# Kernel tuning notes

Hardware: AMD Instinct MI355X
Metric: run time of the kernel (lower is better)

Reference implementation:

```python
import jax, jax.numpy as jnp
import numpy as np

N = 100_000   # nodes
E = 1_600_000 # edges (avg degree 16)
D = 128       # dim == dim_out
NEG_SLOPE = 0.2  # PyG GATConv default


def setup_inputs() -> dict:
    key = jax.random.key(0)
    ks = jax.random.split(key, 11)
    s = 1.0 / np.sqrt(D)
    return {
        "x": jax.random.normal(ks[0], (N, D), jnp.float32),
        "edge_index": jax.random.randint(ks[1], (2, E), 0, N, jnp.int32),
        "W1": jax.random.normal(ks[2], (D, D), jnp.float32) * s,
        "a_src1": jax.random.normal(ks[3], (D,), jnp.float32) * s,
        "a_dst1": jax.random.normal(ks[4], (D,), jnp.float32) * s,
        "b1": jnp.zeros((D,), jnp.float32),
        "W2": jax.random.normal(ks[5], (D, D), jnp.float32) * s,
        "a_src2": jax.random.normal(ks[6], (D,), jnp.float32) * s,
        "a_dst2": jax.random.normal(ks[7], (D,), jnp.float32) * s,
        "b2": jnp.zeros((D,), jnp.float32),
    }


def gat_conv(x, W, a_src, a_dst, b, src, dst, n):
    # PyG GATConv, heads=1: message flows src (j) -> dst (i)
    h = x @ W                              # [n, d]
    al_src = h @ a_src                     # per-node src attention logit
    al_dst = h @ a_dst                     # per-node dst attention logit
    e = jax.nn.leaky_relu(al_src[src] + al_dst[dst], NEG_SLOPE)  # [E']
    # softmax over incoming edges of each destination node (segment softmax)
    m = jax.ops.segment_max(e, dst, num_segments=n)
    e = jnp.exp(e - m[dst])
    z = jax.ops.segment_sum(e, dst, num_segments=n)
    alpha = e / z[dst]                     # [E']
    out = jax.ops.segment_sum(h[src] * alpha[:, None], dst, num_segments=n)
    return out + b


def reference(x, edge_index, W1, a_src1, a_dst1, b1, W2, a_src2, a_dst2, b2):
    n = x.shape[0]
    loop = jnp.arange(n, dtype=edge_index.dtype)
    src = jnp.concatenate([edge_index[0], loop])  # add_self_loops=True
    dst = jnp.concatenate([edge_index[1], loop])
    h = gat_conv(x, W1, a_src1, a_dst1, b1, src, dst, n)
    # self_loops=True -> residual=False; dropout in eval mode = identity
    return gat_conv(h, W2, a_src2, a_dst2, b2, src, dst, n)
```

## Files before the change

### kernel.cpp

```cpp
#include <hip/hip_runtime.h>
#include <hip/hip_bf16.h>
#include <math.h>

#define D 128
#define LRELU_SLOPE 0.2f
#define BSH 9
#define BSZ 512
#define SC_CHUNK 16384

typedef __attribute__((ext_vector_type(8))) short bf16x8;
typedef __attribute__((ext_vector_type(4))) float f32x4;

__device__ __forceinline__ float lrelu(float x){ return x > 0.f ? x : LRELU_SLOPE * x; }

__device__ __forceinline__ unsigned short bf16_rn(float x){
  unsigned int u = __float_as_uint(x);
  return (unsigned short)((u + 0x7FFFu + ((u >> 16) & 1u)) >> 16);
}
__device__ __forceinline__ float bf16_lo_f(unsigned int u){ return __uint_as_float(u << 16); }
__device__ __forceinline__ float bf16_hi_f(unsigned int u){ return __uint_as_float(u & 0xFFFF0000u); }

__global__ __launch_bounds__(1024) void bucket_count_kernel(const int* __restrict__ dst, int E,
    int* __restrict__ bcnt, int nbuck){
  __shared__ int h[256];
  int t = threadIdx.x;
  if (t < 256) h[t] = 0;
  __syncthreads();
  for (int e = blockIdx.x*1024 + t; e < E; e += gridDim.x*1024)
    atomicAdd(&h[dst[e] >> BSH], 1);
  __syncthreads();
  if (t < nbuck && h[t]) atomicAdd(&bcnt[t], h[t]);
}

__global__ __launch_bounds__(256) void bucket_scan_kernel(const int* __restrict__ bcnt,
    int* __restrict__ bbase, int* __restrict__ bcur, int nbuck, int E){
  __shared__ int s[256];
  int t = threadIdx.x;
  int v = (t < nbuck) ? bcnt[t] : 0;
  s[t] = v;
  __syncthreads();
  #pragma unroll
  for (int d = 1; d < 256; d <<= 1){
    int add = (t >= d) ? s[t-d] : 0;
    __syncthreads();
    s[t] += add;
    __syncthreads();
  }
  if (t < nbuck){ int b = s[t] - v; bbase[t] = b; bcur[t] = b; }
  if (t == 0) bbase[nbuck] = E;
}

__global__ __launch_bounds__(1024) void bucket_scatter_kernel(const int* __restrict__ src,
    const int* __restrict__ dst, int E, int* __restrict__ bcur,
    unsigned int* __restrict__ ebuf, int nbuck){
  __shared__ int h[256];
  __shared__ int cb[256];
  int t = threadIdx.x;
  int base = blockIdx.x * SC_CHUNK;
  int end = base + SC_CHUNK; if (end > E) end = E;
  if (t < 256) h[t] = 0;
  __syncthreads();
  for (int e = base + t; e < end; e += 1024)
    atomicAdd(&h[dst[e] >> BSH], 1);
  __syncthreads();
  if (t < nbuck){
    cb[t] = h[t] ? atomicAdd(&bcur[t], h[t]) : 0;
    h[t] = 0;
  }
  __syncthreads();
  for (int e = base + t; e < end; e += 1024){
    int d = dst[e];
    int b = d >> BSH;
    int lpos = atomicAdd(&h[b], 1);
    ebuf[cb[b] + lpos] = ((unsigned int)src[e] << BSH) | (unsigned int)(d & (BSZ-1));
  }
}

__global__ __launch_bounds__(256) void bucket_csr_kernel(const unsigned int* __restrict__ ebuf,
    const int* __restrict__ bbase, int* __restrict__ row_ptr, int* __restrict__ col,
    int n, int nbuck){
  __shared__ int c[512];
  __shared__ int ps[256];
  int b = blockIdx.x;
  int t = threadIdx.x;
  int base = bbase[b], end = bbase[b+1];
  c[t] = 0; c[t+256] = 0;
  __syncthreads();
  for (int i = base + t; i < end; i += 256)
    atomicAdd(&c[ebuf[i] & (BSZ-1)], 1);
  __syncthreads();
  int a0 = c[2*t], a1 = c[2*t+1];
  int pair = a0 + a1;
  ps[t] = pair;
  __syncthreads();
  #pragma unroll
  for (int d = 1; d < 256; d <<= 1){
    int add = (t >= d) ? ps[t-d] : 0;
    __syncthreads();
    ps[t] += add;
    __syncthreads();
  }
  int excl = ps[t] - pair;
  __syncthreads();
  int lo = b << BSH;
  int g0 = lo + 2*t, g1 = g0 + 1;
  if (g0 < n) row_ptr[g0] = base + excl;
  if (g1 < n) row_ptr[g1] = base + excl + a0;
  c[2*t]   = excl;
  c[2*t+1] = excl + a0;
  __syncthreads();
  for (int i = base + t; i < end; i += 256){
    unsigned int p = ebuf[i];
    int dlo = p & (BSZ-1);
    int pos = base + atomicAdd(&c[dlo], 1);
    col[pos] = (int)(p >> BSH);
  }
  if (b == 0 && t == 0) row_ptr[n] = bbase[nbuck];
}

__global__ __launch_bounds__(256) void wsplit_kernel(const float* __restrict__ W,
    unsigned short* __restrict__ Whf, unsigned short* __restrict__ Wlf){
  int t = blockIdx.x*256 + threadIdx.x;
  int k  = t >> 7;
  int nn = t & 127;
  float w = W[t];
  unsigned short h = bf16_rn(w);
  float whf = __uint_as_float(((unsigned int)h) << 16);
  unsigned short l = bf16_rn(w - whf);
  int kc = k >> 5, l4 = (k >> 3) & 3, e = k & 7;
  int cf = nn >> 4, l15 = nn & 15;
  int idx = ((kc*8 + cf)*64 + l4*16 + l15)*8 + e;
  Whf[idx] = h; Wlf[idx] = l;
}

__global__ __launch_bounds__(64) void wa_kernel(const float* __restrict__ W,
    const float* __restrict__ a_src, const float* __restrict__ a_dst,
    float* __restrict__ wa_s, float* __restrict__ wa_d){
  int task = blockIdx.x;
  int row = task & 127;
  const float* a = (task >> 7) ? a_dst : a_src;
  int l = threadIdx.x;
  float2 v = ((const float2*)(W + row*D))[l];
  float p = v.x*a[2*l] + v.y*a[2*l+1];
  #pragma unroll
  for (int off = 32; off >= 1; off >>= 1) p += __shfl_xor(p, off);
  if (l == 0) ((task >> 7) ? wa_d : wa_s)[row] = p;
}

__global__ __launch_bounds__(256) void wafrag_kernel(const float* __restrict__ wa_s,
    const float* __restrict__ wa_d, unsigned short* __restrict__ Whfx,
    unsigned short* __restrict__ Wlfx){
  int t = threadIdx.x;
  int kc = t >> 6, lane = t & 63;
  int l15 = lane & 15, l4 = lane >> 4;
  unsigned short hh[8], ll[8];
  #pragma unroll
  for (int e = 0; e < 8; ++e){
    int k = (kc*4 + l4)*8 + e;
    float v = (l15 == 0) ? wa_s[k] : ((l15 == 1) ? wa_d[k] : 0.f);
    unsigned short h = bf16_rn(v);
    hh[e] = h;
    ll[e] = bf16_rn(v - __uint_as_float(((unsigned)h) << 16));
  }
  #pragma unroll
  for (int e = 0; e < 8; ++e){ Whfx[t*8 + e] = hh[e]; Wlfx[t*8 + e] = ll[e]; }
}

__global__ __launch_bounds__(256) void gemm_al_kernel(const float* __restrict__ X,
    const unsigned short* __restrict__ Whf, const unsigned short* __restrict__ Wlf,
    const unsigned short* __restrict__ Whfx, const unsigned short* __restrict__ Wlfx,
    unsigned short* __restrict__ Hb, float* __restrict__ ALs, float* __restrict__ ALd, int n)
{
  __shared__ unsigned short Xh[128*128];
  int tid  = threadIdx.x;
  int lane = tid & 63;
  int wave = tid >> 6;
  int row0 = blockIdx.x * 128;
  int c4   = tid & 31;

  #pragma unroll 4
  for (int it = 0; it < 16; ++it){
    int f  = it*256 + tid;
    int r  = f >> 5;
    float4 v = make_float4(0.f,0.f,0.f,0.f);
    int gr = row0 + r;
    if (gr < n) v = ((const float4*)(X + (size_t)gr*D))[c4];
    unsigned short h0 = bf16_rn(v.x);
    unsigned short h1 = bf16_rn(v.y);
    unsigned short h2 = bf16_rn(v.z);
    unsigned short h3 = bf16_rn(v.w);
    int g   = (c4 >> 1) ^ (r & 7);
    int idx = r*128 + (g << 3) + ((c4 & 1) << 2);
    *(uint2*)&Xh[idx] = make_uint2((unsigned)h0 | ((unsigned)h1<<16),
                                   (unsigned)h2 | ((unsigned)h3<<16));
  }
  __syncthreads();

  int l15 = lane & 15;
  int l4  = lane >> 4;

  f32x4 acc[2][8];
  f32x4 acc2[2];
  #pragma unroll
  for (int rf = 0; rf < 2; ++rf){
    #pragma unroll
    for (int cf = 0; cf < 8; ++cf)
      acc[rf][cf] = (f32x4){0.f, 0.f, 0.f, 0.f};
    acc2[rf] = (f32x4){0.f, 0.f, 0.f, 0.f};
  }

  #pragma unroll
  for (int kc = 0; kc < 4; ++kc){
    int g = kc*4 + l4;
    bf16x8 ah[2];
    #pragma unroll
    for (int rf = 0; rf < 2; ++rf){
      int r   = wave*32 + rf*16 + l15;
      int idx = r*128 + ((g ^ (r & 7)) << 3);
      ah[rf] = *(const bf16x8*)&Xh[idx];
    }
    #pragma unroll
    for (int cf = 0; cf < 8; ++cf){
      int foff = ((kc*8 + cf) << 9) + (lane << 3);
      bf16x8 bh = *(const bf16x8*)&Whf[foff];
      bf16x8 bl = *(const bf16x8*)&Wlf[foff];
      #pragma unroll
      for (int rf = 0; rf < 2; ++rf){
        acc[rf][cf] = __builtin_amdgcn_mfma_f32_16x16x32_bf16(ah[rf], bh, acc[rf][cf], 0, 0, 0);
        acc[rf][cf] = __builtin_amdgcn_mfma_f32_16x16x32_bf16(ah[rf], bl, acc[rf][cf], 0, 0, 0);
      }
    }
    {
      int foffx = ((kc << 6) + lane) << 3;
      bf16x8 bhx = *(const bf16x8*)&Whfx[foffx];
      bf16x8 blx = *(const bf16x8*)&Wlfx[foffx];
      #pragma unroll
      for (int rf = 0; rf < 2; ++rf){
        acc2[rf] = __builtin_amdgcn_mfma_f32_16x16x32_bf16(ah[rf], bhx, acc2[rf], 0, 0, 0);
        acc2[rf] = __builtin_amdgcn_mfma_f32_16x16x32_bf16(ah[rf], blx, acc2[rf], 0, 0, 0);
      }
    }
  }

  #pragma unroll
  for (int rf = 0; rf < 2; ++rf){
    #pragma unroll
    for (int reg = 0; reg < 4; ++reg){
      int gr = row0 + wave*32 + rf*16 + l4*4 + reg;
      if (gr < n){
        unsigned int p0 = (unsigned)bf16_rn(acc[rf][0][reg]) | ((unsigned)bf16_rn(acc[rf][1][reg]) << 16);
        unsigned int p1 = (unsigned)bf16_rn(acc[rf][2][reg]) | ((unsigned)bf16_rn(acc[rf][3][reg]) << 16);
        unsigned int p2 = (unsigned)bf16_rn(acc[rf][4][reg]) | ((unsigned)bf16_rn(acc[rf][5][reg]) << 16);
        unsigned int p3 = (unsigned)bf16_rn(acc[rf][6][reg]) | ((unsigned)bf16_rn(acc[rf][7][reg]) << 16);
        ((uint4*)(Hb + (size_t)gr*D))[l15] = make_uint4(p0, p1, p2, p3);
        if (l15 == 0)      ALs[gr] = acc2[rf][reg];
        else if (l15 == 1) ALd[gr] = acc2[rf][reg];
      }
    }
  }
}

__global__ __launch_bounds__(256) void agg_kernel(const unsigned short* __restrict__ Hb,
    const float* __restrict__ ALs, const float* __restrict__ ALd,
    const int* __restrict__ row_ptr, const int* __restrict__ col,
    const float* __restrict__ bias, float* __restrict__ out, int n)
{
  __shared__ uint2 pairs[256];
  int gtid = blockIdx.x*blockDim.x + threadIdx.x;
  int node = gtid >> 6;
  int lane = threadIdx.x & 63;
  int wbase = threadIdx.x & 192;
  if (node >= n) return;

  int beg = row_ptr[node], end = row_ptr[node+1];
  float ald = ALd[node];
  float e_self = lrelu(ALs[node] + ald);

  const unsigned int* H2 = (const unsigned int*)Hb;
  unsigned int us = H2[(unsigned)(node*64 + lane)];
  float2 acc; acc.x = bf16_lo_f(us); acc.y = bf16_hi_f(us);
  float m = e_self, z = 1.f;

  for (int c = beg; c < end; c += 64){
    int j = c + lane;
    bool valid = j < end;
    int s_l = valid ? col[j] : 0;
    float e_l = valid ? lrelu(ALs[s_l] + ald) : -1e30f;

    float mc = e_l;
    #pragma unroll
    for (int off = 32; off >= 1; off >>= 1) mc = fmaxf(mc, __shfl_xor(mc, off));
    if (mc > m){
      float sc = __expf(m - mc);
      z *= sc; acc.x *= sc; acc.y *= sc;
      m = mc;
    }
    float w_l = valid ? __expf(e_l - m) : 0.f;
    float zs = w_l;
    #pragma unroll
    for (int off = 32; off >= 1; off >>= 1) zs += __shfl_xor(zs, off);
    z += zs;

    pairs[threadIdx.x] = make_uint2((unsigned)s_l, __float_as_uint(w_l));

    int cnt = end - c; if (cnt > 64) cnt = 64;
    int q = 0;
    for (; q + 8 <= cnt; q += 8){
      uint2 pw[8]; unsigned int u[8];
      #pragma unroll
      for (int p = 0; p < 8; ++p) pw[p] = pairs[wbase + q + p];
      #pragma unroll
      for (int p = 0; p < 8; ++p) u[p] = H2[(unsigned)(pw[p].x*64u + lane)];
      #pragma unroll
      for (int p = 0; p < 8; ++p){
        float w = __uint_as_float(pw[p].y);
        acc.x += w*bf16_lo_f(u[p]);
        acc.y += w*bf16_hi_f(u[p]);
      }
    }
    for (; q < cnt; ++q){
      uint2 pw = pairs[wbase + q];
      unsigned int u = H2[(unsigned)(pw.x*64u + lane)];
      float w = __uint_as_float(pw.y);
      acc.x += w*bf16_lo_f(u); acc.y += w*bf16_hi_f(u);
    }
  }

  float zi = 1.f / z;
  acc.x *= zi; acc.y *= zi;

  int q0 = (lane >> 4) + ((lane & 7) << 3);
  int q1 = q0 + 4;
  int hsel = (lane >> 3) & 1;
  float x0 = __shfl(acc.x, q0), y0 = __shfl(acc.y, q0);
  float x1 = __shfl(acc.x, q1), y1 = __shfl(acc.y, q1);
  float v0 = hsel ? y0 : x0;
  float v1 = hsel ? y1 : x1;

  float2 b2 = ((const float2*)bias)[lane];
  ((float2*)out)[(size_t)node*64 + lane] = make_float2(v0 + b2.x, v1 + b2.y);
}

extern "C" void kernel_launch(void* const* d_in, const int* in_sizes, int n_in,
                              void* d_out, int out_size, void* d_ws, size_t ws_size,
                              hipStream_t stream)
{
  const float* x   = (const float*)d_in[0];
  const int*   ei  = (const int*)  d_in[1];
  const float* W1  = (const float*)d_in[2];
  const float* as1 = (const float*)d_in[3];
  const float* ad1 = (const float*)d_in[4];
  const float* b1  = (const float*)d_in[5];
  const float* W2  = (const float*)d_in[6];
  const float* as2 = (const float*)d_in[7];
  const float* ad2 = (const float*)d_in[8];
  const float* b2  = (const float*)d_in[9];

  int n = in_sizes[0] / D;
  int E = in_sizes[1] / 2;
  const int* src = ei;
  const int* dst = ei + E;
  int nbuck = (n + BSZ - 1) >> BSH;

  char* base = (char*)d_ws;
  size_t off = 0;
  auto alloc = [&](size_t bytes) -> char* {
    char* p = base + off;
    off = (off + bytes + 255) & ~(size_t)255;
    return p;
  };
  unsigned short* hb = (unsigned short*)alloc((size_t)n*D*2);
  float* als   = (float*)alloc((size_t)n*4);
  float* ald   = (float*)alloc((size_t)n*4);
  int* row_ptr = (int*)alloc((size_t)(n+1)*4);
  int* bcnt    = (int*)alloc(256*4);
  int* bbase   = (int*)alloc(257*4);
  int* bcur    = (int*)alloc(256*4);
  unsigned short* whf1 = (unsigned short*)alloc(16384*2);
  unsigned short* wlf1 = (unsigned short*)alloc(16384*2);
  unsigned short* whf2 = (unsigned short*)alloc(16384*2);
  unsigned short* wlf2 = (unsigned short*)alloc(16384*2);
  unsigned short* whfx1 = (unsigned short*)alloc(2048*2);
  unsigned short* wlfx1 = (unsigned short*)alloc(2048*2);
  unsigned short* whfx2 = (unsigned short*)alloc(2048*2);
  unsigned short* wlfx2 = (unsigned short*)alloc(2048*2);
  float* wa_s1 = (float*)alloc(128*4);
  float* wa_d1 = (float*)alloc(128*4);
  float* wa_s2 = (float*)alloc(128*4);
  float* wa_d2 = (float*)alloc(128*4);
  unsigned int* ebuf = (unsigned int*)alloc((size_t)E*4);
  int* col   = (int*)alloc((size_t)E*4);

  float* out = (float*)d_out;

  hipMemsetAsync(bcnt, 0, 256*sizeof(int), stream);
  int sc_blocks = (E + SC_CHUNK - 1) / SC_CHUNK;
  bucket_count_kernel  <<<128, 1024, 0, stream>>>(dst, E, bcnt, nbuck);
  bucket_scan_kernel   <<<1, 256, 0, stream>>>(bcnt, bbase, bcur, nbuck, E);
  bucket_scatter_kernel<<<sc_blocks, 1024, 0, stream>>>(src, dst, E, bcur, ebuf, nbuck);
  bucket_csr_kernel    <<<nbuck, 256, 0, stream>>>(ebuf, bbase, row_ptr, col, n, nbuck);

  wsplit_kernel<<<64, 256, 0, stream>>>(W1, whf1, wlf1);
  wsplit_kernel<<<64, 256, 0, stream>>>(W2, whf2, wlf2);
  wa_kernel    <<<256, 64, 0, stream>>>(W1, as1, ad1, wa_s1, wa_d1);
  wa_kernel    <<<256, 64, 0, stream>>>(W2, as2, ad2, wa_s2, wa_d2);
  wafrag_kernel<<<1, 256, 0, stream>>>(wa_s1, wa_d1, whfx1, wlfx1);
  wafrag_kernel<<<1, 256, 0, stream>>>(wa_s2, wa_d2, whfx2, wlfx2);

  int ntiles = (n + 127)/128;
  int aggblocks = (int)(((size_t)n*64 + 255)/256);

  gemm_al_kernel<<<ntiles, 256, 0, stream>>>(x,  whf1, wlf1, whfx1, wlfx1, hb, als, ald, n);
  agg_kernel    <<<aggblocks, 256, 0, stream>>>(hb, als, ald, row_ptr, col, b1, out, n);
  gemm_al_kernel<<<ntiles, 256, 0, stream>>>(out, whf2, wlf2, whfx2, wlfx2, hb, als, ald, n);
  agg_kernel    <<<aggblocks, 256, 0, stream>>>(hb, als, ald, row_ptr, col, b2, out, n);
}
```

Measured before the change: 290.8 us.

## Replace online softmax max with global upper-bound shift from per-node logit maxima

Adds a small reduction kernel that computes the global maxima of the source and destination attention logits. The aggregation kernel then uses lrelu(max_src+max_dst) as a fixed shift, which is a valid upper bound because leaky ReLU is monotone. This removes the per-chunk wave max reduction, the rescaling branch and the per-chunk sum reduction, leaving one sum reduction at the end. The cost is an extra kernel launch plus memsets per layer, and a risk of underflow when a node's logits sit far below the global maximum.

```diff
diff --git a/kernel.cpp b/kernel.cpp
--- a/kernel.cpp
+++ b/kernel.cpp
@@ -19,6 +19,14 @@
 }
 __device__ __forceinline__ float bf16_lo_f(unsigned int u){ return __uint_as_float(u << 16); }
 __device__ __forceinline__ float bf16_hi_f(unsigned int u){ return __uint_as_float(u & 0xFFFF0000u); }
+
+__device__ __forceinline__ unsigned int enc_f(float f){
+  unsigned int u = __float_as_uint(f);
+  return (u & 0x80000000u) ? ~u : (u | 0x80000000u);
+}
+__device__ __forceinline__ float dec_f(unsigned int e){
+  return __uint_as_float((e & 0x80000000u) ? (e & 0x7FFFFFFFu) : ~e);
+}
 
 __global__ __launch_bounds__(1024) void bucket_count_kernel(const int* __restrict__ dst, int E,
     int* __restrict__ bcnt, int nbuck){
@@ -164,6 +172,25 @@
   }
   #pragma unroll
   for (int e = 0; e < 8; ++e){ Whfx[t*8 + e] = hh[e]; Wlfx[t*8 + e] = ll[e]; }
+}
+
+__global__ __launch_bounds__(256) void almax_kernel(const float* __restrict__ als,
+    const float* __restrict__ ald, unsigned int* __restrict__ mx, int n){
+  int t = blockIdx.x*256 + threadIdx.x;
+  float ms = -1e30f, md = -1e30f;
+  for (int i = t; i < n; i += gridDim.x*256){
+    ms = fmaxf(ms, als[i]);
+    md = fmaxf(md, ald[i]);
+  }
+  #pragma unroll
+  for (int off = 32; off >= 1; off >>= 1){
+    ms = fmaxf(ms, __shfl_xor(ms, off));
+    md = fmaxf(md, __shfl_xor(md, off));
+  }
+  if ((threadIdx.x & 63) == 0){
+    atomicMax(&mx[0], enc_f(ms));
+    atomicMax(&mx[1], enc_f(md));
+  }
 }
 
 __global__ __launch_bounds__(256) void gemm_al_kernel(const float* __restrict__ X,
@@ -262,6 +289,7 @@
 
 __global__ __launch_bounds__(256) void agg_kernel(const unsigned short* __restrict__ Hb,
     const float* __restrict__ ALs, const float* __restrict__ ALd,
+    const unsigned int* __restrict__ mx,
     const int* __restrict__ row_ptr, const int* __restrict__ col,
     const float* __restrict__ bias, float* __restrict__ out, int n)
 {
@@ -272,34 +300,23 @@
   int wbase = threadIdx.x & 192;
   if (node >= n) return;
 
+  float M = lrelu(dec_f(mx[0]) + dec_f(mx[1]));
+
   int beg = row_ptr[node], end = row_ptr[node+1];
   float ald = ALd[node];
-  float e_self = lrelu(ALs[node] + ald);
+  float ws = __expf(lrelu(ALs[node] + ald) - M);
 
   const unsigned int* H2 = (const unsigned int*)Hb;
   unsigned int us = H2[(unsigned)(node*64 + lane)];
-  float2 acc; acc.x = bf16_lo_f(us); acc.y = bf16_hi_f(us);
-  float m = e_self, z = 1.f;
+  float2 acc; acc.x = ws * bf16_lo_f(us); acc.y = ws * bf16_hi_f(us);
+  float zl = 0.f;
 
   for (int c = beg; c < end; c += 64){
     int j = c + lane;
     bool valid = j < end;
     int s_l = valid ? col[j] : 0;
-    float e_l = valid ? lrelu(ALs[s_l] + ald) : -1e30f;
-
-    float mc = e_l;
-    #pragma unroll
-    for (int off = 32; off >= 1; off >>= 1) mc = fmaxf(mc, __shfl_xor(mc, off));
-    if (mc > m){
-      float sc = __expf(m - mc);
-      z *= sc; acc.x *= sc; acc.y *= sc;
-      m = mc;
-    }
-    float w_l = valid ? __expf(e_l - m) : 0.f;
-    float zs = w_l;
-    #pragma unroll
-    for (int off = 32; off >= 1; off >>= 1) zs += __shfl_xor(zs, off);
-    z += zs;
+    float w_l = valid ? __expf(lrelu(ALs[s_l] + ald) - M) : 0.f;
+    zl += w_l;
 
     pairs[threadIdx.x] = make_uint2((unsigned)s_l, __float_as_uint(w_l));
 
@@ -326,7 +343,9 @@
     }
   }
 
-  float zi = 1.f / z;
+  #pragma unroll
+  for (int off = 32; off >= 1; off >>= 1) zl += __shfl_xor(zl, off);
+  float zi = 1.f / (zl + ws);
   acc.x *= zi; acc.y *= zi;
 
   int q0 = (lane >> 4) + ((lane & 7) << 3);
@@ -376,6 +395,8 @@
   int* bcnt    = (int*)alloc(256*4);
   int* bbase   = (int*)alloc(257*4);
   int* bcur    = (int*)alloc(256*4);
+  unsigned int* mx1 = (unsigned int*)alloc(2*4);
+  unsigned int* mx2 = (unsigned int*)alloc(2*4);
   unsigned short* whf1 = (unsigned short*)alloc(16384*2);
   unsigned short* wlf1 = (unsigned short*)alloc(16384*2);
   unsigned short* whf2 = (unsigned short*)alloc(16384*2);
@@ -394,6 +415,9 @@
   float* out = (float*)d_out;
 
   hipMemsetAsync(bcnt, 0, 256*sizeof(int), stream);
+  hipMemsetAsync(mx1, 0, 2*sizeof(unsigned int), stream);
+  hipMemsetAsync(mx2, 0, 2*sizeof(unsigned int), stream);
+
   int sc_blocks = (E + SC_CHUNK - 1) / SC_CHUNK;
   bucket_count_kernel  <<<128, 1024, 0, stream>>>(dst, E, bcnt, nbuck);
   bucket_scan_kernel   <<<1, 256, 0, stream>>>(bcnt, bbase, bcur, nbuck, E);
@@ -411,7 +435,9 @@
   int aggblocks = (int)(((size_t)n*64 + 255)/256);
 
   gemm_al_kernel<<<ntiles, 256, 0, stream>>>(x,  whf1, wlf1, whfx1, wlfx1, hb, als, ald, n);
-  agg_kernel    <<<aggblocks, 256, 0, stream>>>(hb, als, ald, row_ptr, col, b1, out, n);
+  almax_kernel  <<<128, 256, 0, stream>>>(als, ald, mx1, n);
+  agg_kernel    <<<aggblocks, 256, 0, stream>>>(hb, als, ald, mx1, row_ptr, col, b1, out, n);
   gemm_al_kernel<<<ntiles, 256, 0, stream>>>(out, whf2, wlf2, whfx2, wlfx2, hb, als, ald, n);
-  agg_kernel    <<<aggblocks, 256, 0, stream>>>(hb, als, ald, row_ptr, col, b2, out, n);
-}
+  almax_kernel  <<<128, 256, 0, stream>>>(als, ald, mx2, n);
+  agg_kernel    <<<aggblocks, 256, 0, stream>>>(hb, als, ald, mx2, row_ptr, col, b2, out, n);
+}
```

New measurement: 313.3 us. +7.7%, slower.
